# Performance work log

Measured on AMD Instinct MI355X. Metric: run time of the kernel, lower is better.

The kernel has to match this reference:

```python
import jax, jax.numpy as jnp
import numpy as np

E, D, MULT, K = 8, 1024, 4, 2   # num_experts, hidden_dim, mlp_multiplier, top-k
B, S = 4, 2048
H = MULT * D


def setup_inputs() -> dict:
    key = jax.random.key(0)
    k0, k1, k2, k3 = jax.random.split(key, 4)
    x = jax.random.normal(k0, (B, S, D), dtype=jnp.float32)
    Wr = jax.random.normal(k1, (E, D), dtype=jnp.float32) * (D ** -0.5)        # router (no bias)
    W1 = jax.random.normal(k2, (E, D, H), dtype=jnp.float32) * (D ** -0.5)     # expert fc1
    b1 = jnp.zeros((E, H), dtype=jnp.float32)
    W2 = jax.random.normal(k3, (E, H, D), dtype=jnp.float32) * (H ** -0.5)     # expert fc2
    b2 = jnp.zeros((E, D), dtype=jnp.float32)
    return {"x": x, "Wr": Wr, "W1": W1, "b1": b1, "W2": W2, "b2": b2}


def reference(x, Wr, W1, b1, W2, b2):
    # Router: softmax over experts then top-k -> per-token combine weights.
    probs = jax.nn.softmax(jnp.einsum("bsd,ed->bse", x, Wr), axis=-1)  # [B,S,E]
    topv, topi = jax.lax.top_k(probs, K)                                # [B,S,K]
    # combine[b,s,e] = sum_k topv * 1[topi==e]  (same math as the masked scatter-add)
    combine = jnp.sum(topv[..., None] * jax.nn.one_hot(topi, E, dtype=x.dtype), axis=2)  # [B,S,E]

    def body(acc, params):
        w1, bb1, w2, bb2, ce = params  # ce: [B,S] combine weight for this expert
        h = jax.nn.gelu(jnp.einsum("bsd,dh->bsh", x, w1) + bb1, approximate=False)
        y = jnp.einsum("bsh,hd->bsd", h, w2) + bb2
        return acc + ce[..., None] * y, None

    cE = jnp.moveaxis(combine, -1, 0)  # [E,B,S]
    out, _ = jax.lax.scan(body, jnp.zeros_like(x), (W1, b1, W2, b2, cE))
    return out
```

## Files before the change

kernel.cpp:

```cpp
#include <hip/hip_runtime.h>
#include <hip/hip_bf16.h>

#define E_   8
#define D_   1024
#define H_   4096
#define T_   8192
#define TM   128
#define BK   64
#define CAP  17408
#define NBY  136
#define CK   2

typedef __attribute__((ext_vector_type(8))) short short8;
typedef __attribute__((ext_vector_type(4))) float floatx4;

__device__ __forceinline__ unsigned short f2bf(float f) {
    unsigned u = __float_as_uint(f);
    u += 0x7fffu + ((u >> 16) & 1u);
    return (unsigned short)(u >> 16);
}
__device__ __forceinline__ float bf2f(unsigned short u) {
    return __uint_as_float((unsigned)u << 16);
}

#define GLP16(g, l)                                                             \
    __builtin_amdgcn_global_load_lds((const __attribute__((address_space(1))) void*)(g), \
                                     (__attribute__((address_space(3))) void*)(l), 16, 0, 0)

__global__ __launch_bounds__(64) void router_kernel(
    const float* __restrict__ x, const float* __restrict__ Wr,
    int* __restrict__ cnt, int* __restrict__ tok_list,
    int2* __restrict__ inv_ei, float2* __restrict__ inv_w)
{
    int t = blockIdx.x;
    int lane = threadIdx.x;
    const float* xr = x + (size_t)t * D_;
    float acc[E_];
#pragma unroll
    for (int e = 0; e < E_; ++e) acc[e] = 0.f;
    for (int it = 0; it < D_ / 64; ++it) {
        float xv = xr[lane + it * 64];
#pragma unroll
        for (int e = 0; e < E_; ++e) acc[e] += xv * Wr[e * D_ + lane + it * 64];
    }
#pragma unroll
    for (int e = 0; e < E_; ++e) {
#pragma unroll
        for (int off = 32; off; off >>= 1) acc[e] += __shfl_xor(acc[e], off);
    }
    if (lane == 0) {
        float m = acc[0];
#pragma unroll
        for (int e = 1; e < E_; ++e) m = fmaxf(m, acc[e]);
        float p[E_]; float s = 0.f;
#pragma unroll
        for (int e = 0; e < E_; ++e) { p[e] = expf(acc[e] - m); s += p[e]; }
        float inv = 1.f / s;
        int i1 = 0; float v1 = p[0];
#pragma unroll
        for (int e = 1; e < E_; ++e) if (p[e] > v1) { v1 = p[e]; i1 = e; }
        int i2 = -1; float v2 = -1.f;
#pragma unroll
        for (int e = 0; e < E_; ++e) { if (e == i1) continue; if (p[e] > v2) { v2 = p[e]; i2 = e; } }
        v1 *= inv; v2 *= inv;
        int pos1 = atomicAdd(&cnt[i1], 1);
        tok_list[i1 * T_ + pos1] = t;
        int pos2 = atomicAdd(&cnt[i2], 1);
        tok_list[i2 * T_ + pos2] = t;
        inv_ei[t] = make_int2(i1 | (pos1 << 3), i2 | (pos2 << 3));
        inv_w[t] = make_float2(v1, v2);
    }
}

__global__ void offsets_kernel(const int* __restrict__ cnt, int* __restrict__ start)
{
    if (threadIdx.x == 0) {
        int s = 0;
        for (int e = 0; e < E_; ++e) {
            start[e] = s;
            s += (cnt[e] + TM - 1) / TM * TM;
        }
        start[E_] = s;
    }
}

__global__ __launch_bounds__(256) void gather_kernel(
    const float* __restrict__ x, const int* __restrict__ cnt, const int* __restrict__ start,
    const int* __restrict__ tok_list, unsigned short* __restrict__ xg)
{
    int row = blockIdx.x;
    int tid = threadIdx.x;
    int tot = start[E_];
    if (row >= tot) return;
    int e = 0;
    while (e < E_ - 1 && row >= start[e + 1]) ++e;
    int idx = row - start[e];
    unsigned short* dst = xg + (size_t)row * D_;
    if (idx < cnt[e]) {
        int t = tok_list[e * T_ + idx];
        const float4* src = (const float4*)(x + (size_t)t * D_);
        float4 v = src[tid];
        ushort4 o; o.x = f2bf(v.x); o.y = f2bf(v.y); o.z = f2bf(v.z); o.w = f2bf(v.w);
        ((ushort4*)dst)[tid] = o;
    } else {
        ((ushort4*)dst)[tid] = make_ushort4(0, 0, 0, 0);
    }
}

__global__ __launch_bounds__(256) void transpose_cvt(
    const float* __restrict__ in, unsigned short* __restrict__ out, int R, int C)
{
    __shared__ float tile[32][33];
    int e = blockIdx.z;
    int c0 = blockIdx.x * 32, r0 = blockIdx.y * 32;
    const float* src = in + (size_t)e * R * C;
    unsigned short* dst = out + (size_t)e * R * C;
    int tx = threadIdx.x & 31, ty = threadIdx.x >> 5;
#pragma unroll
    for (int i = 0; i < 32; i += 8)
        tile[ty + i][tx] = src[(size_t)(r0 + ty + i) * C + c0 + tx];
    __syncthreads();
#pragma unroll
    for (int i = 0; i < 32; i += 8)
        dst[(size_t)(c0 + ty + i) * R + r0 + tx] = f2bf(tile[tx][ty + i]);
}

__global__ __launch_bounds__(256) void fc1_kernel(
    const unsigned short* __restrict__ xg, const unsigned short* __restrict__ w1t,
    const float* __restrict__ b1, const int* __restrict__ start, unsigned short* __restrict__ h)
{
    __shared__ __align__(16) unsigned short Asm[TM * BK];
    __shared__ __align__(16) unsigned short Bsm[TM * BK];

    int row0 = blockIdx.y * TM;
    int tot = start[E_];
    if (row0 >= tot) return;
    int e = 0;
    while (e < E_ - 1 && row0 >= start[e + 1]) ++e;

    int n0 = blockIdx.x * TM;
    const unsigned short* Ag = xg + (size_t)row0 * D_;
    const unsigned short* Bg = w1t + (size_t)e * H_ * D_ + (size_t)n0 * D_;

    int tid = threadIdx.x;
    int wid = tid >> 6, lane = tid & 63;
    int wm = wid >> 1, wn = wid & 1;
    int quad = lane >> 4, r16 = lane & 15;
    int srow = (lane >> 3);
    int scol = ((lane & 7) ^ srow) * 8;
    int rsw = r16 & 7;

    floatx4 acc[4][4];
#pragma unroll
    for (int i = 0; i < 4; ++i)
#pragma unroll
        for (int j = 0; j < 4; ++j) acc[i][j] = (floatx4){0.f, 0.f, 0.f, 0.f};

    for (int kc = 0; kc < D_ / BK; ++kc) {
        int k0 = kc * BK;
#pragma unroll
        for (int q = 0; q < 4; ++q) {
            int rb = wid * 32 + q * 8;
            GLP16(Ag + (size_t)(rb + srow) * D_ + k0 + scol, Asm + rb * BK);
            GLP16(Bg + (size_t)(rb + srow) * D_ + k0 + scol, Bsm + rb * BK);
        }
        __syncthreads();
#pragma unroll
        for (int ks = 0; ks < 2; ++ks) {
            short8 af[4], bfr[4];
#pragma unroll
            for (int i = 0; i < 4; ++i)
                af[i] = *(const short8*)(Asm + (wm * 64 + i * 16 + r16) * BK + ((ks * 4 + quad) ^ rsw) * 8);
#pragma unroll
            for (int j = 0; j < 4; ++j)
                bfr[j] = *(const short8*)(Bsm + (wn * 64 + j * 16 + r16) * BK + ((ks * 4 + quad) ^ rsw) * 8);
#pragma unroll
            for (int i = 0; i < 4; ++i)
#pragma unroll
                for (int j = 0; j < 4; ++j)
                    acc[i][j] = __builtin_amdgcn_mfma_f32_16x16x32_bf16(af[i], bfr[j], acc[i][j], 0, 0, 0);
        }
        __syncthreads();
    }

    const float* b1e = b1 + (size_t)e * H_;
    float bj[4];
#pragma unroll
    for (int j = 0; j < 4; ++j) bj[j] = b1e[n0 + wn * 64 + j * 16 + r16];
#pragma unroll
    for (int i = 0; i < 4; ++i) {
#pragma unroll
        for (int r = 0; r < 4; ++r) {
            size_t rowg = (size_t)row0 + wm * 64 + i * 16 + quad * 4 + r;
            unsigned short* hp = h + rowg * H_ + n0 + wn * 64 + r16;
#pragma unroll
            for (int j = 0; j < 4; ++j) {
                float v = acc[i][j][r] + bj[j];
                float u = 1.5957691f * v * fmaf(0.044715f, v * v, 1.f);
                float g = v * __builtin_amdgcn_rcpf(1.f + __expf(-u));
                hp[j * 16] = f2bf(g);
            }
        }
    }
}

__global__ __launch_bounds__(256) void fc2_kernel(
    const unsigned short* __restrict__ h, const unsigned short* __restrict__ w2t,
    const int* __restrict__ start, unsigned short* __restrict__ y)
{
    __shared__ __align__(16) unsigned short Asm[TM * BK];
    __shared__ __align__(16) unsigned short Bsm[TM * BK];

    int row0 = blockIdx.y * TM;
    int tot = start[E_];
    if (row0 >= tot) return;
    int e = 0;
    while (e < E_ - 1 && row0 >= start[e + 1]) ++e;

    int n0 = blockIdx.x * TM;
    const unsigned short* Ag = h + (size_t)row0 * H_;
    const unsigned short* Bg = w2t + (size_t)e * D_ * H_ + (size_t)n0 * H_;

    int tid = threadIdx.x;
    int wid = tid >> 6, lane = tid & 63;
    int wm = wid >> 1, wn = wid & 1;
    int quad = lane >> 4, r16 = lane & 15;
    int srow = (lane >> 3);
    int scol = ((lane & 7) ^ srow) * 8;
    int rsw = r16 & 7;

    floatx4 acc[4][4];
#pragma unroll
    for (int i = 0; i < 4; ++i)
#pragma unroll
        for (int j = 0; j < 4; ++j) acc[i][j] = (floatx4){0.f, 0.f, 0.f, 0.f};

    const int KITERS = H_ / BK / CK;
    int kbase = blockIdx.z * KITERS;
    for (int kc = kbase; kc < kbase + KITERS; ++kc) {
        int k0 = kc * BK;
#pragma unroll
        for (int q = 0; q < 4; ++q) {
            int rb = wid * 32 + q * 8;
            GLP16(Ag + (size_t)(rb + srow) * H_ + k0 + scol, Asm + rb * BK);
            GLP16(Bg + (size_t)(rb + srow) * H_ + k0 + scol, Bsm + rb * BK);
        }
        __syncthreads();
#pragma unroll
        for (int ks = 0; ks < 2; ++ks) {
            short8 af[4], bfr[4];
#pragma unroll
            for (int i = 0; i < 4; ++i)
                af[i] = *(const short8*)(Asm + (wm * 64 + i * 16 + r16) * BK + ((ks * 4 + quad) ^ rsw) * 8);
#pragma unroll
            for (int j = 0; j < 4; ++j)
                bfr[j] = *(const short8*)(Bsm + (wn * 64 + j * 16 + r16) * BK + ((ks * 4 + quad) ^ rsw) * 8);
#pragma unroll
            for (int i = 0; i < 4; ++i)
#pragma unroll
                for (int j = 0; j < 4; ++j)
                    acc[i][j] = __builtin_amdgcn_mfma_f32_16x16x32_bf16(af[i], bfr[j], acc[i][j], 0, 0, 0);
        }
        __syncthreads();
    }

    unsigned short* ys = y + (size_t)blockIdx.z * CAP * D_;
#pragma unroll
    for (int i = 0; i < 4; ++i) {
#pragma unroll
        for (int r = 0; r < 4; ++r) {
            int row = row0 + wm * 64 + i * 16 + quad * 4 + r;
            unsigned short* op = ys + (size_t)row * D_ + n0 + wn * 64 + r16;
#pragma unroll
            for (int j = 0; j < 4; ++j)
                op[j * 16] = f2bf(acc[i][j][r]);
        }
    }
}

__global__ __launch_bounds__(256) void combine_kernel(
    const unsigned short* __restrict__ y, const int* __restrict__ start,
    const int2* __restrict__ inv_ei, const float2* __restrict__ inv_w,
    const float* __restrict__ b2, float* __restrict__ out)
{
    int t = blockIdx.x;
    int tid = threadIdx.x;
    int2 ei = inv_ei[t];
    float2 w = inv_w[t];
    int e1 = ei.x & 7, x1 = ei.x >> 3;
    int e2 = ei.y & 7, x2 = ei.y >> 3;
    size_t r1 = (size_t)start[e1] + x1;
    size_t r2 = (size_t)start[e2] + x2;
    const size_t SL = (size_t)CAP * D_;
    ushort4 a0 = ((const ushort4*)(y + r1 * D_))[tid];
    ushort4 a1 = ((const ushort4*)(y + SL + r1 * D_))[tid];
    ushort4 c0 = ((const ushort4*)(y + r2 * D_))[tid];
    ushort4 c1 = ((const ushort4*)(y + SL + r2 * D_))[tid];
    float4 bA = ((const float4*)(b2 + (size_t)e1 * D_))[tid];
    float4 bB = ((const float4*)(b2 + (size_t)e2 * D_))[tid];
    float4 o;
    o.x = w.x * (bf2f(a0.x) + bf2f(a1.x) + bA.x) + w.y * (bf2f(c0.x) + bf2f(c1.x) + bB.x);
    o.y = w.x * (bf2f(a0.y) + bf2f(a1.y) + bA.y) + w.y * (bf2f(c0.y) + bf2f(c1.y) + bB.y);
    o.z = w.x * (bf2f(a0.z) + bf2f(a1.z) + bA.z) + w.y * (bf2f(c0.z) + bf2f(c1.z) + bB.z);
    o.w = w.x * (bf2f(a0.w) + bf2f(a1.w) + bA.w) + w.y * (bf2f(c0.w) + bf2f(c1.w) + bB.w);
    ((float4*)(out + (size_t)t * D_))[tid] = o;
}

extern "C" void kernel_launch(void* const* d_in, const int* in_sizes, int n_in,
                              void* d_out, int out_size, void* d_ws, size_t ws_size,
                              hipStream_t stream)
{
    const float* x  = (const float*)d_in[0];
    const float* Wr = (const float*)d_in[1];
    const float* W1 = (const float*)d_in[2];
    const float* b1 = (const float*)d_in[3];
    const float* W2 = (const float*)d_in[4];
    const float* b2 = (const float*)d_in[5];
    float* out = (float*)d_out;

    char* ws = (char*)d_ws;
    int*    cnt      = (int*)ws;
    int*    start    = (int*)(ws + 64);
    int*    tok_list = (int*)(ws + 256);
    int2*   inv_ei   = (int2*)(ws + 393216);
    float2* inv_w    = (float2*)(ws + 458752);
    char* p0 = ws + (1u << 20);
    unsigned short* xg  = (unsigned short*)p0;
    unsigned short* w1t = (unsigned short*)(p0 + 35651584ull);
    unsigned short* h   = (unsigned short*)(p0 + 35651584ull + 67108864ull);
    unsigned short* w2t = (unsigned short*)(p0 + 35651584ull + 67108864ull + 142606336ull);
    unsigned short* y   = (unsigned short*)p0;
    (void)ws_size; (void)in_sizes; (void)n_in; (void)out_size;

    hipMemsetAsync(ws, 0, 64, stream);

    transpose_cvt<<<dim3(H_ / 32, D_ / 32, E_), 256, 0, stream>>>(W1, w1t, D_, H_);
    transpose_cvt<<<dim3(D_ / 32, H_ / 32, E_), 256, 0, stream>>>(W2, w2t, H_, D_);
    router_kernel<<<T_, 64, 0, stream>>>(x, Wr, cnt, tok_list, inv_ei, inv_w);
    offsets_kernel<<<1, 64, 0, stream>>>(cnt, start);
    gather_kernel<<<CAP, 256, 0, stream>>>(x, cnt, start, tok_list, xg);
    fc1_kernel<<<dim3(H_ / TM, NBY), 256, 0, stream>>>(xg, w1t, b1, start, h);
    fc2_kernel<<<dim3(D_ / TM, NBY, CK), 256, 0, stream>>>(h, w2t, start, y);
    combine_kernel<<<T_, 256, 0, stream>>>(y, start, inv_ei, inv_w, b2, out);
}
```

Baseline: 971.4 us.

## Switch expert GEMMs to 32x32x16 MFMA with 128x256 tiles, merge weight transposes

Both expert GEMMs move from 16x16x32 MFMA on 128x128 tiles with 4 waves to 32x32x16 MFMA on 128x256 tiles with 8 waves, each wave holding a 2x2 grid of 32x32 accumulators. The two weight transpose/convert launches become one launch using 64x64 tiles and float4 loads. The aim is better MFMA throughput per LDS read and more reuse of the A tile, paid for with more LDS per block and a changed output scatter pattern.

```diff
diff --git a/kernel.cpp b/kernel.cpp
--- a/kernel.cpp
+++ b/kernel.cpp
@@ -5,14 +5,15 @@
 #define D_   1024
 #define H_   4096
 #define T_   8192
-#define TM   128
+#define TMM  128
+#define TNN  256
 #define BK   64
 #define CAP  17408
 #define NBY  136
 #define CK   2
 
 typedef __attribute__((ext_vector_type(8))) short short8;
-typedef __attribute__((ext_vector_type(4))) float floatx4;
+typedef __attribute__((ext_vector_type(16))) float floatx16;
 
 __device__ __forceinline__ unsigned short f2bf(float f) {
     unsigned u = __float_as_uint(f);
@@ -78,7 +79,7 @@
         int s = 0;
         for (int e = 0; e < E_; ++e) {
             start[e] = s;
-            s += (cnt[e] + TM - 1) / TM * TM;
+            s += (cnt[e] + TMM - 1) / TMM * TMM;
         }
         start[E_] = s;
     }
@@ -108,172 +109,201 @@
 }
 
 __global__ __launch_bounds__(256) void transpose_cvt(
-    const float* __restrict__ in, unsigned short* __restrict__ out, int R, int C)
-{
-    __shared__ float tile[32][33];
-    int e = blockIdx.z;
-    int c0 = blockIdx.x * 32, r0 = blockIdx.y * 32;
-    const float* src = in + (size_t)e * R * C;
-    unsigned short* dst = out + (size_t)e * R * C;
-    int tx = threadIdx.x & 31, ty = threadIdx.x >> 5;
-#pragma unroll
-    for (int i = 0; i < 32; i += 8)
-        tile[ty + i][tx] = src[(size_t)(r0 + ty + i) * C + c0 + tx];
+    const float* __restrict__ W1, const float* __restrict__ W2,
+    unsigned short* __restrict__ w1t, unsigned short* __restrict__ w2t)
+{
+    __shared__ float tile[64][65];
+    int z = blockIdx.z;
+    const float* src; unsigned short* dst; int R, C, r0, c0;
+    if (z < 8) {
+        src = W1 + (size_t)z * D_ * H_;       dst = w1t + (size_t)z * D_ * H_;
+        R = D_; C = H_; r0 = blockIdx.y * 64; c0 = blockIdx.x * 64;
+    } else {
+        src = W2 + (size_t)(z - 8) * H_ * D_; dst = w2t + (size_t)(z - 8) * H_ * D_;
+        R = H_; C = D_; r0 = blockIdx.x * 64; c0 = blockIdx.y * 64;
+    }
+    int t = threadIdx.x;
+    int r = t >> 4, c4 = (t & 15) * 4;
+#pragma unroll
+    for (int p = 0; p < 4; ++p) {
+        int row = p * 16 + r;
+        float4 v = *(const float4*)(src + (size_t)(r0 + row) * C + c0 + c4);
+        tile[row][c4 + 0] = v.x; tile[row][c4 + 1] = v.y;
+        tile[row][c4 + 2] = v.z; tile[row][c4 + 3] = v.w;
+    }
     __syncthreads();
 #pragma unroll
-    for (int i = 0; i < 32; i += 8)
-        dst[(size_t)(c0 + ty + i) * R + r0 + tx] = f2bf(tile[tx][ty + i]);
-}
-
-__global__ __launch_bounds__(256) void fc1_kernel(
+    for (int p = 0; p < 4; ++p) {
+        int orow = p * 16 + r;
+        ushort4 o;
+        o.x = f2bf(tile[c4 + 0][orow]); o.y = f2bf(tile[c4 + 1][orow]);
+        o.z = f2bf(tile[c4 + 2][orow]); o.w = f2bf(tile[c4 + 3][orow]);
+        *(ushort4*)(dst + (size_t)(c0 + orow) * R + r0 + c4) = o;
+    }
+}
+
+__global__ __launch_bounds__(512) void fc1_kernel(
     const unsigned short* __restrict__ xg, const unsigned short* __restrict__ w1t,
     const float* __restrict__ b1, const int* __restrict__ start, unsigned short* __restrict__ h)
 {
-    __shared__ __align__(16) unsigned short Asm[TM * BK];
-    __shared__ __align__(16) unsigned short Bsm[TM * BK];
-
-    int row0 = blockIdx.y * TM;
+    __shared__ __align__(16) unsigned short Asm[TMM * BK];
+    __shared__ __align__(16) unsigned short Bsm[TNN * BK];
+
+    int row0 = blockIdx.y * TMM;
     int tot = start[E_];
     if (row0 >= tot) return;
     int e = 0;
     while (e < E_ - 1 && row0 >= start[e + 1]) ++e;
 
-    int n0 = blockIdx.x * TM;
+    int n0 = blockIdx.x * TNN;
     const unsigned short* Ag = xg + (size_t)row0 * D_;
     const unsigned short* Bg = w1t + (size_t)e * H_ * D_ + (size_t)n0 * D_;
 
     int tid = threadIdx.x;
     int wid = tid >> 6, lane = tid & 63;
-    int wm = wid >> 1, wn = wid & 1;
-    int quad = lane >> 4, r16 = lane & 15;
-    int srow = (lane >> 3);
+    int wm = wid & 1, wn = wid >> 1;
+    int m31 = lane & 31, khalf = lane >> 5;
+    int srow = lane >> 3;
     int scol = ((lane & 7) ^ srow) * 8;
-    int rsw = r16 & 7;
-
-    floatx4 acc[4][4];
-#pragma unroll
-    for (int i = 0; i < 4; ++i)
-#pragma unroll
-        for (int j = 0; j < 4; ++j) acc[i][j] = (floatx4){0.f, 0.f, 0.f, 0.f};
+
+    floatx16 acc[2][2];
+#pragma unroll
+    for (int i = 0; i < 2; ++i)
+#pragma unroll
+        for (int j = 0; j < 2; ++j)
+#pragma unroll
+            for (int r = 0; r < 16; ++r) acc[i][j][r] = 0.f;
 
     for (int kc = 0; kc < D_ / BK; ++kc) {
         int k0 = kc * BK;
 #pragma unroll
+        for (int q = 0; q < 2; ++q) {
+            int rb = wid * 16 + q * 8;
+            GLP16(Ag + (size_t)(rb + srow) * D_ + k0 + scol, Asm + rb * BK);
+        }
+#pragma unroll
         for (int q = 0; q < 4; ++q) {
             int rb = wid * 32 + q * 8;
-            GLP16(Ag + (size_t)(rb + srow) * D_ + k0 + scol, Asm + rb * BK);
             GLP16(Bg + (size_t)(rb + srow) * D_ + k0 + scol, Bsm + rb * BK);
         }
         __syncthreads();
 #pragma unroll
-        for (int ks = 0; ks < 2; ++ks) {
-            short8 af[4], bfr[4];
-#pragma unroll
-            for (int i = 0; i < 4; ++i)
-                af[i] = *(const short8*)(Asm + (wm * 64 + i * 16 + r16) * BK + ((ks * 4 + quad) ^ rsw) * 8);
-#pragma unroll
-            for (int j = 0; j < 4; ++j)
-                bfr[j] = *(const short8*)(Bsm + (wn * 64 + j * 16 + r16) * BK + ((ks * 4 + quad) ^ rsw) * 8);
-#pragma unroll
-            for (int i = 0; i < 4; ++i)
-#pragma unroll
-                for (int j = 0; j < 4; ++j)
-                    acc[i][j] = __builtin_amdgcn_mfma_f32_16x16x32_bf16(af[i], bfr[j], acc[i][j], 0, 0, 0);
+        for (int ks = 0; ks < 4; ++ks) {
+            int g = ((ks * 2 + khalf) ^ (lane & 7)) * 8;
+            short8 af[2], bfr[2];
+#pragma unroll
+            for (int i = 0; i < 2; ++i)
+                af[i] = *(const short8*)(Asm + (wm * 64 + i * 32 + m31) * BK + g);
+#pragma unroll
+            for (int j = 0; j < 2; ++j)
+                bfr[j] = *(const short8*)(Bsm + (wn * 64 + j * 32 + m31) * BK + g);
+#pragma unroll
+            for (int i = 0; i < 2; ++i)
+#pragma unroll
+                for (int j = 0; j < 2; ++j)
+                    acc[i][j] = __builtin_amdgcn_mfma_f32_32x32x16_bf16(af[i], bfr[j], acc[i][j], 0, 0, 0);
         }
         __syncthreads();
     }
 
     const float* b1e = b1 + (size_t)e * H_;
-    float bj[4];
-#pragma unroll
-    for (int j = 0; j < 4; ++j) bj[j] = b1e[n0 + wn * 64 + j * 16 + r16];
-#pragma unroll
-    for (int i = 0; i < 4; ++i) {
-#pragma unroll
-        for (int r = 0; r < 4; ++r) {
-            size_t rowg = (size_t)row0 + wm * 64 + i * 16 + quad * 4 + r;
-            unsigned short* hp = h + rowg * H_ + n0 + wn * 64 + r16;
-#pragma unroll
-            for (int j = 0; j < 4; ++j) {
-                float v = acc[i][j][r] + bj[j];
+    int colb = n0 + wn * 64 + m31;
+    float bb[2] = { b1e[colb], b1e[colb + 32] };
+#pragma unroll
+    for (int i = 0; i < 2; ++i) {
+        int rb = row0 + wm * 64 + i * 32 + 4 * khalf;
+#pragma unroll
+        for (int j = 0; j < 2; ++j) {
+#pragma unroll
+            for (int reg = 0; reg < 16; ++reg) {
+                int row = rb + (reg & 3) + 8 * (reg >> 2);
+                float v = acc[i][j][reg] + bb[j];
                 float u = 1.5957691f * v * fmaf(0.044715f, v * v, 1.f);
-                float g = v * __builtin_amdgcn_rcpf(1.f + __expf(-u));
-                hp[j * 16] = f2bf(g);
+                float gl = v * __builtin_amdgcn_rcpf(1.f + __expf(-u));
+                h[(size_t)row * H_ + colb + j * 32] = f2bf(gl);
             }
         }
     }
 }
 
-__global__ __launch_bounds__(256) void fc2_kernel(
+__global__ __launch_bounds__(512) void fc2_kernel(
     const unsigned short* __restrict__ h, const unsigned short* __restrict__ w2t,
     const int* __restrict__ start, unsigned short* __restrict__ y)
 {
-    __shared__ __align__(16) unsigned short Asm[TM * BK];
-    __shared__ __align__(16) unsigned short Bsm[TM * BK];
-
-    int row0 = blockIdx.y * TM;
+    __shared__ __align__(16) unsigned short Asm[TMM * BK];
+    __shared__ __align__(16) unsigned short Bsm[TNN * BK];
+
+    int row0 = blockIdx.y * TMM;
     int tot = start[E_];
     if (row0 >= tot) return;
     int e = 0;
     while (e < E_ - 1 && row0 >= start[e + 1]) ++e;
 
-    int n0 = blockIdx.x * TM;
+    int n0 = blockIdx.x * TNN;
     const unsigned short* Ag = h + (size_t)row0 * H_;
     const unsigned short* Bg = w2t + (size_t)e * D_ * H_ + (size_t)n0 * H_;
 
     int tid = threadIdx.x;
     int wid = tid >> 6, lane = tid & 63;
-    int wm = wid >> 1, wn = wid & 1;
-    int quad = lane >> 4, r16 = lane & 15;
-    int srow = (lane >> 3);
+    int wm = wid & 1, wn = wid >> 1;
+    int m31 = lane & 31, khalf = lane >> 5;
+    int srow = lane >> 3;
     int scol = ((lane & 7) ^ srow) * 8;
-    int rsw = r16 & 7;
-
-    floatx4 acc[4][4];
-#pragma unroll
-    for (int i = 0; i < 4; ++i)
-#pragma unroll
-        for (int j = 0; j < 4; ++j) acc[i][j] = (floatx4){0.f, 0.f, 0.f, 0.f};
+
+    floatx16 acc[2][2];
+#pragma unroll
+    for (int i = 0; i < 2; ++i)
+#pragma unroll
+        for (int j = 0; j < 2; ++j)
+#pragma unroll
+            for (int r = 0; r < 16; ++r) acc[i][j][r] = 0.f;
 
     const int KITERS = H_ / BK / CK;
     int kbase = blockIdx.z * KITERS;
     for (int kc = kbase; kc < kbase + KITERS; ++kc) {
         int k0 = kc * BK;
 #pragma unroll
+        for (int q = 0; q < 2; ++q) {
+            int rb = wid * 16 + q * 8;
+            GLP16(Ag + (size_t)(rb + srow) * H_ + k0 + scol, Asm + rb * BK);
+        }
+#pragma unroll
         for (int q = 0; q < 4; ++q) {
             int rb = wid * 32 + q * 8;
-            GLP16(Ag + (size_t)(rb + srow) * H_ + k0 + scol, Asm + rb * BK);
             GLP16(Bg + (size_t)(rb + srow) * H_ + k0 + scol, Bsm + rb * BK);
         }
         __syncthreads();
 #pragma unroll
-        for (int ks = 0; ks < 2; ++ks) {
-            short8 af[4], bfr[4];
-#pragma unroll
-            for (int i = 0; i < 4; ++i)
-                af[i] = *(const short8*)(Asm + (wm * 64 + i * 16 + r16) * BK + ((ks * 4 + quad) ^ rsw) * 8);
-#pragma unroll
-            for (int j = 0; j < 4; ++j)
-                bfr[j] = *(const short8*)(Bsm + (wn * 64 + j * 16 + r16) * BK + ((ks * 4 + quad) ^ rsw) * 8);
-#pragma unroll
-            for (int i = 0; i < 4; ++i)
-#pragma unroll
-                for (int j = 0; j < 4; ++j)
-                    acc[i][j] = __builtin_amdgcn_mfma_f32_16x16x32_bf16(af[i], bfr[j], acc[i][j], 0, 0, 0);
+        for (int ks = 0; ks < 4; ++ks) {
+            int g = ((ks * 2 + khalf) ^ (lane & 7)) * 8;
+            short8 af[2], bfr[2];
+#pragma unroll
+            for (int i = 0; i < 2; ++i)
+                af[i] = *(const short8*)(Asm + (wm * 64 + i * 32 + m31) * BK + g);
+#pragma unroll
+            for (int j = 0; j < 2; ++j)
+                bfr[j] = *(const short8*)(Bsm + (wn * 64 + j * 32 + m31) * BK + g);
+#pragma unroll
+            for (int i = 0; i < 2; ++i)
+#pragma unroll
+                for (int j = 0; j < 2; ++j)
+                    acc[i][j] = __builtin_amdgcn_mfma_f32_32x32x16_bf16(af[i], bfr[j], acc[i][j], 0, 0, 0);
         }
         __syncthreads();
     }
 
     unsigned short* ys = y + (size_t)blockIdx.z * CAP * D_;
-#pragma unroll
-    for (int i = 0; i < 4; ++i) {
-#pragma unroll
-        for (int r = 0; r < 4; ++r) {
-            int row = row0 + wm * 64 + i * 16 + quad * 4 + r;
-            unsigned short* op = ys + (size_t)row * D_ + n0 + wn * 64 + r16;
-#pragma unroll
-            for (int j = 0; j < 4; ++j)
-                op[j * 16] = f2bf(acc[i][j][r]);
+    int colb = n0 + wn * 64 + m31;
+#pragma unroll
+    for (int i = 0; i < 2; ++i) {
+        int rb = row0 + wm * 64 + i * 32 + 4 * khalf;
+#pragma unroll
+        for (int j = 0; j < 2; ++j) {
+#pragma unroll
+            for (int reg = 0; reg < 16; ++reg) {
+                int row = rb + (reg & 3) + 8 * (reg >> 2);
+                ys[(size_t)row * D_ + colb + j * 32] = f2bf(acc[i][j][reg]);
+            }
         }
     }
 }
@@ -334,12 +364,11 @@
 
     hipMemsetAsync(ws, 0, 64, stream);
 
-    transpose_cvt<<<dim3(H_ / 32, D_ / 32, E_), 256, 0, stream>>>(W1, w1t, D_, H_);
-    transpose_cvt<<<dim3(D_ / 32, H_ / 32, E_), 256, 0, stream>>>(W2, w2t, H_, D_);
+    transpose_cvt<<<dim3(64, 16, 16), 256, 0, stream>>>(W1, W2, w1t, w2t);
     router_kernel<<<T_, 64, 0, stream>>>(x, Wr, cnt, tok_list, inv_ei, inv_w);
     offsets_kernel<<<1, 64, 0, stream>>>(cnt, start);
     gather_kernel<<<CAP, 256, 0, stream>>>(x, cnt, start, tok_list, xg);
-    fc1_kernel<<<dim3(H_ / TM, NBY), 256, 0, stream>>>(xg, w1t, b1, start, h);
-    fc2_kernel<<<dim3(D_ / TM, NBY, CK), 256, 0, stream>>>(h, w2t, start, y);
+    fc1_kernel<<<dim3(H_ / TNN, NBY), 512, 0, stream>>>(xg, w1t, b1, start, h);
+    fc2_kernel<<<dim3(D_ / TNN, NBY, CK), 512, 0, stream>>>(h, w2t, start, y);
     combine_kernel<<<T_, 256, 0, stream>>>(y, start, inv_ei, inv_w, b2, out);
 }
```

After: 930.7 us. 4.2% less time.
